# Kernel tuning notes

Hardware: AMD Instinct MI355X
Metric: run time of the kernel (lower is better)

Reference implementation:

```python
import jax, jax.numpy as jnp
import numpy as np

N = 100000
E = 1600000
D_IN = 128
D_OUT = 128

def setup_inputs() -> dict:
    key = jax.random.key(0)
    ks = jax.random.split(key, 8)
    x = jax.random.normal(ks[0], (N, D_IN), dtype=jnp.float32)
    edge_index = jax.random.randint(ks[1], (2, E), 0, N, dtype=jnp.int64)
    s = 1.0 / np.sqrt(D_IN)
    W_l = jax.random.uniform(ks[2], (D_OUT, D_IN), minval=-s, maxval=s, dtype=jnp.float32)
    b_l = jax.random.uniform(ks[3], (D_OUT,), minval=-s, maxval=s, dtype=jnp.float32)
    W_r = jax.random.uniform(ks[4], (D_OUT, D_IN), minval=-s, maxval=s, dtype=jnp.float32)
    gamma = jnp.ones((D_OUT,), dtype=jnp.float32)
    beta = jnp.zeros((D_OUT,), dtype=jnp.float32)
    return {"x": x, "edge_index": edge_index, "W_l": W_l, "b_l": b_l,
            "W_r": W_r, "gamma": gamma, "beta": beta}

def reference(x, edge_index, W_l, b_l, W_r, gamma, beta):
    src, dst = edge_index[0], edge_index[1]
    # mean-aggregate neighbor features: gather src features, scatter-sum to dst
    msg = x[src]                                             # [E, D_IN]
    agg = jax.ops.segment_sum(msg, dst, num_segments=N)      # [N, D_IN]
    deg = jax.ops.segment_sum(jnp.ones((E,), x.dtype), dst, num_segments=N)
    agg = agg / jnp.maximum(deg, 1.0)[:, None]               # nodes w/o neighbors -> 0
    # SAGEConv: lin_l(aggregated) + lin_r(root)
    out = agg @ W_l.T + b_l + x @ W_r.T                      # [N, D_OUT]
    # LayerNorm over feature dim
    mu = jnp.mean(out, axis=-1, keepdims=True)
    var = jnp.var(out, axis=-1, keepdims=True)
    out = (out - mu) * jax.lax.rsqrt(var + 1e-5) * gamma + beta
    # ReLU; dropout in eval mode is identity
    return jax.nn.relu(out)
```

## Files before the change

kernel.cpp:

```cpp
#include <hip/hip_runtime.h>


#define D 128
#define SCAN_NB 256
#define NPB 256
#define MAXNB 1024
#define SLAB 4608
#define NCONV 2048

typedef __attribute__((ext_vector_type(8))) short bf16x8;
typedef __attribute__((ext_vector_type(4))) float f32x4;

__device__ inline unsigned short f2bf(float f) {
    unsigned int u = __builtin_bit_cast(unsigned int, f);
    u += 0x7FFFu + ((u >> 16) & 1u);
    return (unsigned short)(u >> 16);
}
__device__ inline float bf_lo(unsigned int u) {
    return __builtin_bit_cast(float, u << 16);
}
__device__ inline float bf_hi(unsigned int u) {
    return __builtin_bit_cast(float, u & 0xFFFF0000u);
}

__global__ void slab_init(int* __restrict__ bcur, int nb) {
    int b = blockIdx.x * blockDim.x + threadIdx.x;
    if (b < nb) bcur[b] = b * SLAB;
}

__global__ __launch_bounds__(256) void bin_kernel(const int* __restrict__ ei,
                                                  int* __restrict__ bcur,
                                                  unsigned int* __restrict__ staged,
                                                  int n_edges, int nb) {
    __shared__ int hist[MAXNB];
    __shared__ int base[MAXNB];
    int tid = threadIdx.x;
    for (int i = tid; i < nb; i += 256) hist[i] = 0;
    __syncthreads();
    int chunk = (n_edges + gridDim.x - 1) / gridDim.x;
    int e0 = blockIdx.x * chunk, e1 = min(e0 + chunk, n_edges);
    const int* dstp = ei + n_edges;
    for (int e = e0 + tid; e < e1; e += 256)
        atomicAdd(&hist[dstp[e] >> 8], 1);
    __syncthreads();
    for (int i = tid; i < nb; i += 256) {
        int c = hist[i];
        base[i] = c ? atomicAdd(&bcur[i], c) : 0;
        hist[i] = 0;
    }
    __syncthreads();
    for (int e = e0 + tid; e < e1; e += 256) {
        int dst = dstp[e];
        int b = dst >> 8;
        int pos = base[b] + atomicAdd(&hist[b], 1);
        staged[pos] = ((unsigned int)(dst & 255) << 24) | (unsigned int)ei[e];
    }
}

__global__ __launch_bounds__(256) void fill2_slab(const unsigned int* __restrict__ staged,
                                                  const int* __restrict__ bcur,
                                                  int* __restrict__ offs,
                                                  int* __restrict__ deg,
                                                  int* __restrict__ csr, int n_nodes) {
    __shared__ int hist[NPB];
    __shared__ int scn[NPB];
    int b = blockIdx.x;
    int n0 = b << 8;
    int nn = min(NPB, n_nodes - n0);
    int tid = threadIdx.x;
    int base = b * SLAB;
    int cnt = bcur[b] - base;

    hist[tid] = 0;
    __syncthreads();
    for (int e = tid; e < cnt; e += 256)
        atomicAdd(&hist[staged[base + e] >> 24], 1);
    __syncthreads();
    int h = hist[tid];
    scn[tid] = h;
    __syncthreads();
    for (int off = 1; off < 256; off <<= 1) {
        int t = (tid >= off) ? scn[tid - off] : 0;
        __syncthreads();
        scn[tid] += t;
        __syncthreads();
    }
    int start = base + scn[tid] - h;
    if (tid < nn) { offs[n0 + tid] = start; deg[n0 + tid] = h; }
    scn[tid] = start;
    __syncthreads();
    for (int e = tid; e < cnt; e += 256) {
        unsigned int u = staged[base + e];
        int dl = u >> 24;
        int pos = atomicAdd(&scn[dl], 1);
        csr[pos] = (int)(u & 0xFFFFFFu);
    }
}

__global__ __launch_bounds__(256) void prep2_kernel(
        const float* __restrict__ x, unsigned int* __restrict__ xcat, long long n4,
        const float* __restrict__ Wl, const float* __restrict__ Wr,
        bf16x8* __restrict__ wfragg) {
    int b = blockIdx.x;
    int tid = threadIdx.x;
    if (b < NCONV) {
        for (long long i = b * 256LL + tid; i < n4; i += (long long)NCONV * 256) {
            float4 v = reinterpret_cast<const float4*>(x)[i];
            uint2 p;
            p.x = (unsigned int)f2bf(v.x) | ((unsigned int)f2bf(v.y) << 16);
            p.y = (unsigned int)f2bf(v.z) | ((unsigned int)f2bf(v.w) << 16);
            long long row = i >> 5, j = i & 31;
            *reinterpret_cast<uint2*>(xcat + row * 128 + 64 + 2 * j) = p;
        }
    } else {
        int e = (b - NCONV) * 256 + tid;
        int lane = e & 63, kk = (e >> 6) & 7, n0 = e >> 9;
        int dd = n0 * 16 + (lane & 15);
        int k0 = kk * 32 + 8 * (lane >> 4);
        bf16x8 v;
        #pragma unroll
        for (int j = 0; j < 8; ++j) {
            int k = k0 + j;
            float w = (k < 128) ? Wl[dd * 128 + k] : Wr[dd * 128 + (k - 128)];
            v[j] = (short)f2bf(w);
        }
        wfragg[e] = v;
    }
}

__global__ void gather4_kernel(unsigned int* __restrict__ xcat,
                               const int* __restrict__ offs,
                               const int* __restrict__ deg,
                               const int* __restrict__ csr, int n_nodes) {
    int lane = threadIdx.x & 63;
    int col = lane & 15;
    int q   = lane >> 4;
    int gw = (blockIdx.x * blockDim.x + threadIdx.x) >> 6;
    int nw = (gridDim.x * blockDim.x) >> 6;

    for (int node = gw; node < n_nodes; node += nw) {
        int o0 = offs[node], dgi = deg[node], o1 = o0 + dgi;
        float a0 = 0.f, a1 = 0.f, a2 = 0.f, a3 = 0.f,
              a4 = 0.f, a5 = 0.f, a6 = 0.f, a7 = 0.f;
        int i = o0 + q;
        #define LROW(s) (*reinterpret_cast<const uint4*>(xcat + (size_t)(s) * 128 + 64 + (col << 2)))
        #define ACC(u) do { \
            a0 += bf_lo((u).x); a1 += bf_hi((u).x); \
            a2 += bf_lo((u).y); a3 += bf_hi((u).y); \
            a4 += bf_lo((u).z); a5 += bf_hi((u).z); \
            a6 += bf_lo((u).w); a7 += bf_hi((u).w); } while (0)
        for (; i + 12 < o1; i += 16) {
            int s0 = csr[i], s1 = csr[i + 4], s2 = csr[i + 8], s3 = csr[i + 12];
            uint4 u0 = LROW(s0), u1 = LROW(s1), u2 = LROW(s2), u3 = LROW(s3);
            ACC(u0); ACC(u1); ACC(u2); ACC(u3);
        }
        for (; i + 4 < o1; i += 8) {
            int s0 = csr[i], s1 = csr[i + 4];
            uint4 u0 = LROW(s0), u1 = LROW(s1);
            ACC(u0); ACC(u1);
        }
        for (; i < o1; i += 4) {
            uint4 u0 = LROW(csr[i]);
            ACC(u0);
        }
        #undef ACC
        #undef LROW
        a0 += __shfl_xor(a0, 16, 64); a0 += __shfl_xor(a0, 32, 64);
        a1 += __shfl_xor(a1, 16, 64); a1 += __shfl_xor(a1, 32, 64);
        a2 += __shfl_xor(a2, 16, 64); a2 += __shfl_xor(a2, 32, 64);
        a3 += __shfl_xor(a3, 16, 64); a3 += __shfl_xor(a3, 32, 64);
        a4 += __shfl_xor(a4, 16, 64); a4 += __shfl_xor(a4, 32, 64);
        a5 += __shfl_xor(a5, 16, 64); a5 += __shfl_xor(a5, 32, 64);
        a6 += __shfl_xor(a6, 16, 64); a6 += __shfl_xor(a6, 32, 64);
        a7 += __shfl_xor(a7, 16, 64); a7 += __shfl_xor(a7, 32, 64);
        if (q == 0) {
            float inv = 1.0f / fmaxf((float)dgi, 1.0f);
            uint4 p;
            p.x = (unsigned int)f2bf(a0 * inv) | ((unsigned int)f2bf(a1 * inv) << 16);
            p.y = (unsigned int)f2bf(a2 * inv) | ((unsigned int)f2bf(a3 * inv) << 16);
            p.z = (unsigned int)f2bf(a4 * inv) | ((unsigned int)f2bf(a5 * inv) << 16);
            p.w = (unsigned int)f2bf(a6 * inv) | ((unsigned int)f2bf(a7 * inv) << 16);
            *reinterpret_cast<uint4*>(xcat + (size_t)node * 128 + (col << 2)) = p;
        }
    }
}

__global__ __launch_bounds__(256) void sage_mfma3(
        const unsigned int* __restrict__ xcat,
        const bf16x8* __restrict__ wfragg,
        const float* __restrict__ bl,
        const float* __restrict__ gamma,
        const float* __restrict__ beta,
        float* __restrict__ out,
        int n_nodes) {
    __shared__ bf16x8 wf[8 * 8 * 64];

    int tid = threadIdx.x;
    #pragma unroll
    for (int i = 0; i < 16; ++i) wf[i * 256 + tid] = wfragg[i * 256 + tid];
    __syncthreads();

    int wave = tid >> 6, lane = tid & 63;
    int sl = lane & 15, g = lane >> 4;
    int gw = blockIdx.x * 4 + wave;
    int nw = gridDim.x * 4;
    int ndt = (n_nodes + 31) >> 5;

    for (int t = gw; t < ndt; t += nw) {
        int R0 = t << 5;
        int nodeA = R0 + sl;       if (nodeA >= n_nodes) nodeA = n_nodes - 1;
        int nodeB = R0 + 16 + sl;  if (nodeB >= n_nodes) nodeB = n_nodes - 1;
        const bf16x8* arA = reinterpret_cast<const bf16x8*>(xcat) + (size_t)nodeA * 32;
        const bf16x8* arB = reinterpret_cast<const bf16x8*>(xcat) + (size_t)nodeB * 32;

        f32x4 accA[8], accB[8];
        #pragma unroll
        for (int n0 = 0; n0 < 8; ++n0) {
            accA[n0] = (f32x4){0.f, 0.f, 0.f, 0.f};
            accB[n0] = (f32x4){0.f, 0.f, 0.f, 0.f};
        }

        #pragma unroll
        for (int ph = 0; ph < 2; ++ph) {
            bf16x8 vaA[4], vaB[4];
            #pragma unroll
            for (int kk = 0; kk < 4; ++kk) {
                vaA[kk] = arA[ph * 16 + kk * 4 + g];
                vaB[kk] = arB[ph * 16 + kk * 4 + g];
            }
            #pragma unroll
            for (int n0 = 0; n0 < 8; ++n0)
                #pragma unroll
                for (int kk = 0; kk < 4; ++kk) {
                    bf16x8 w = wf[(n0 * 8 + ph * 4 + kk) * 64 + lane];
                    accA[n0] = __builtin_amdgcn_mfma_f32_16x16x32_bf16(vaA[kk], w, accA[n0], 0, 0, 0);
                    accB[n0] = __builtin_amdgcn_mfma_f32_16x16x32_bf16(vaB[kk], w, accB[n0], 0, 0, 0);
                }
        }

        #pragma unroll
        for (int half = 0; half < 2; ++half) {
            f32x4* acc = half ? accB : accA;
            int Rb = R0 + half * 16;
            float s[4] = {0.f, 0.f, 0.f, 0.f}, sq[4] = {0.f, 0.f, 0.f, 0.f};
            #pragma unroll
            for (int n0 = 0; n0 < 8; ++n0) {
                float blv = bl[n0 * 16 + sl];
                #pragma unroll
                for (int r = 0; r < 4; ++r) {
                    float v = acc[n0][r] + blv;
                    acc[n0][r] = v;
                    s[r] += v; sq[r] += v * v;
                }
            }
            #pragma unroll
            for (int off = 1; off <= 8; off <<= 1) {
                #pragma unroll
                for (int r = 0; r < 4; ++r) {
                    s[r]  += __shfl_xor(s[r], off, 64);
                    sq[r] += __shfl_xor(sq[r], off, 64);
                }
            }
            float mu[4], rstd[4];
            #pragma unroll
            for (int r = 0; r < 4; ++r) {
                mu[r] = s[r] * (1.0f / 128.0f);
                float var = sq[r] * (1.0f / 128.0f) - mu[r] * mu[r];
                rstd[r] = rsqrtf(var + 1e-5f);
            }
            #pragma unroll
            for (int n0 = 0; n0 < 8; ++n0) {
                float gm = gamma[n0 * 16 + sl];
                float bt = beta[n0 * 16 + sl];
                #pragma unroll
                for (int r = 0; r < 4; ++r) {
                    int m = Rb + 4 * g + r;
                    if (m < n_nodes) {
                        float o = (acc[n0][r] - mu[r]) * rstd[r] * gm + bt;
                        out[(size_t)m * 128 + n0 * 16 + sl] = fmaxf(o, 0.0f);
                    }
                }
            }
        }
    }
}

__global__ void count_kernel(const int* __restrict__ ei, int* __restrict__ deg, int n_edges) {
    for (int e = blockIdx.x * blockDim.x + threadIdx.x; e < n_edges;
         e += gridDim.x * blockDim.x)
        atomicAdd(&deg[ei[n_edges + e]], 1);
}
__global__ __launch_bounds__(256) void scan_partA(const int* __restrict__ deg,
                                                  int* __restrict__ bsum, int n) {
    __shared__ int red[256];
    int b = blockIdx.x;
    int chunk = (n + SCAN_NB - 1) / SCAN_NB;
    int s0 = b * chunk, s1 = min(s0 + chunk, n);
    int sum = 0;
    for (int i = s0 + threadIdx.x; i < s1; i += 256) sum += deg[i];
    red[threadIdx.x] = sum;
    __syncthreads();
    for (int off = 128; off >= 1; off >>= 1) {
        if (threadIdx.x < off) red[threadIdx.x] += red[threadIdx.x + off];
        __syncthreads();
    }
    if (threadIdx.x == 0) bsum[b] = red[0];
}
__global__ __launch_bounds__(SCAN_NB) void scan_partB(const int* __restrict__ bsum,
                                                      int* __restrict__ boff,
                                                      int* __restrict__ offs, int n) {
    __shared__ int tmp[SCAN_NB];
    int tid = threadIdx.x;
    int v = bsum[tid];
    tmp[tid] = v;
    __syncthreads();
    for (int off = 1; off < SCAN_NB; off <<= 1) {
        int t = (tid >= off) ? tmp[tid - off] : 0;
        __syncthreads();
        tmp[tid] += t;
        __syncthreads();
    }
    boff[tid] = tmp[tid] - v;
    if (tid == SCAN_NB - 1) offs[n] = tmp[tid];
}
__global__ __launch_bounds__(256) void scan_partC(const int* __restrict__ deg,
                                                  const int* __restrict__ boff,
                                                  int* __restrict__ offs,
                                                  int* __restrict__ cursor, int n) {
    __shared__ int tsum[256];
    int b = blockIdx.x;
    int chunk = (n + SCAN_NB - 1) / SCAN_NB;
    int s0 = b * chunk, s1 = min(s0 + chunk, n);
    int tchunk = (chunk + 255) >> 8;
    int t0 = s0 + threadIdx.x * tchunk;
    int t1 = min(t0 + tchunk, s1);
    int sum = 0;
    for (int i = t0; i < t1; ++i) sum += deg[i];
    tsum[threadIdx.x] = sum;
    __syncthreads();
    for (int off = 1; off < 256; off <<= 1) {
        int t = (threadIdx.x >= off) ? tsum[threadIdx.x - off] : 0;
        __syncthreads();
        tsum[threadIdx.x] += t;
        __syncthreads();
    }
    int run = boff[b] + tsum[threadIdx.x] - sum;
    for (int i = t0; i < t1; ++i) {
        offs[i] = run; cursor[i] = run; run += deg[i];
    }
}
__global__ void fill_kernel(const int* __restrict__ ei, int* __restrict__ cursor,
                            int* __restrict__ csr, int n_edges) {
    for (int e = blockIdx.x * blockDim.x + threadIdx.x; e < n_edges;
         e += gridDim.x * blockDim.x) {
        int src = ei[e];
        int dst = ei[n_edges + e];
        int pos = atomicAdd(&cursor[dst], 1);
        csr[pos] = src;
    }
}
__global__ void degfix_kernel(const int* __restrict__ offs, int* __restrict__ deg, int n) {
    for (int i = blockIdx.x * blockDim.x + threadIdx.x; i < n;
         i += gridDim.x * blockDim.x)
        deg[i] = offs[i + 1] - offs[i];
}

__global__ void zero_f(float* __restrict__ a, float* __restrict__ dg, int n_nodes) {
    int total = n_nodes * D + n_nodes;
    for (int i = blockIdx.x * blockDim.x + threadIdx.x; i < total;
         i += gridDim.x * blockDim.x) {
        if (i < n_nodes * D) a[i] = 0.0f;
        else                 dg[i - n_nodes * D] = 0.0f;
    }
}
__global__ void scatter_kernel(const float* __restrict__ x, const int* __restrict__ ei,
                               float* __restrict__ agg, float* __restrict__ deg, int n_edges) {
    long long total = (long long)n_edges * 32;
    for (long long idx = blockIdx.x * (long long)blockDim.x + threadIdx.x; idx < total;
         idx += (long long)gridDim.x * blockDim.x) {
        int e = (int)(idx >> 5);
        int j = (int)(idx & 31);
        int src = ei[e];
        int dst = ei[n_edges + e];
        float4 v = reinterpret_cast<const float4*>(x)[(long long)src * 32 + j];
        float* a = agg + (long long)dst * D + j * 4;
        atomicAdd(a + 0, v.x); atomicAdd(a + 1, v.y);
        atomicAdd(a + 2, v.z); atomicAdd(a + 3, v.w);
        if (j == 0) atomicAdd(deg + dst, 1.0f);
    }
}
__global__ __launch_bounds__(1024) void sage_scalar(
        const float* __restrict__ x, const float* __restrict__ agg_in,
        const float* __restrict__ deg,
        const float* __restrict__ Wl, const float* __restrict__ bl,
        const float* __restrict__ Wr,
        const float* __restrict__ gamma, const float* __restrict__ beta,
        float* __restrict__ out, int n_nodes) {
    __shared__ float wlt[128 * 129];
    __shared__ float wrt[128 * 129];
    __shared__ float rows[16][256];
    int tid = threadIdx.x;
    for (int i = tid; i < 128 * 128; i += 1024) {
        int d = i >> 7, k = i & 127;
        wlt[k * 129 + d] = Wl[i];
        wrt[k * 129 + d] = Wr[i];
    }
    __syncthreads();
    int wave = tid >> 6, lane = tid & 63;
    int gwave = blockIdx.x * 16 + wave;
    int nwaves = gridDim.x * 16;
    float* row = rows[wave];
    int d0 = lane, d1 = lane + 64;
    float bl0 = bl[d0], bl1 = bl[d1];
    float g0 = gamma[d0], g1 = gamma[d1];
    float be0 = beta[d0], be1 = beta[d1];
    for (int n = gwave; n < n_nodes; n += nwaves) {
        float inv = 1.0f / fmaxf(deg[n], 1.0f);
        long long base = (long long)n * D;
        row[lane]       = agg_in[base + lane] * inv;
        row[lane + 64]  = agg_in[base + lane + 64] * inv;
        row[lane + 128] = x[base + lane];
        row[lane + 192] = x[base + lane + 64];
        float acc0 = bl0, acc1 = bl1;
        #pragma unroll 4
        for (int k = 0; k < 128; ++k) {
            float a  = row[k];
            float xv = row[128 + k];
            acc0 += a * wlt[k * 129 + d0];
            acc1 += a * wlt[k * 129 + d1];
            acc0 += xv * wrt[k * 129 + d0];
            acc1 += xv * wrt[k * 129 + d1];
        }
        float s  = acc0 + acc1;
        float sq = acc0 * acc0 + acc1 * acc1;
        #pragma unroll
        for (int off = 32; off >= 1; off >>= 1) {
            s  += __shfl_xor(s, off, 64);
            sq += __shfl_xor(sq, off, 64);
        }
        float mu = s * (1.0f / 128.0f);
        float var = sq * (1.0f / 128.0f) - mu * mu;
        float rstd = rsqrtf(var + 1e-5f);
        float o0 = (acc0 - mu) * rstd * g0 + be0;
        float o1 = (acc1 - mu) * rstd * g1 + be1;
        out[base + d0] = fmaxf(o0, 0.0f);
        out[base + d1] = fmaxf(o1, 0.0f);
    }
}

extern "C" void kernel_launch(void* const* d_in, const int* in_sizes, int n_in,
                              void* d_out, int out_size, void* d_ws, size_t ws_size,
                              hipStream_t stream) {
    const float* x     = (const float*)d_in[0];
    const int*   ei    = (const int*)d_in[1];
    const float* Wl    = (const float*)d_in[2];
    const float* bl    = (const float*)d_in[3];
    const float* Wr    = (const float*)d_in[4];
    const float* gamma = (const float*)d_in[5];
    const float* beta  = (const float*)d_in[6];

    int n_nodes = in_sizes[0] / D;
    int n_edges = in_sizes[1] / 2;
    int nb = (n_nodes + NPB - 1) / NPB;
    int ndt = (n_nodes + 31) >> 5;
    int sage_blocks = (ndt + 3) / 4;

    size_t csr_slab  = (size_t)nb * SLAB;
    size_t csr_leg   = (size_t)n_edges;
    size_t head      = (size_t)n_nodes * 3 + 1 + 2 * SCAN_NB + MAXNB + 16384;
    size_t int_slab  = (head + (csr_slab > csr_leg ? csr_slab : csr_leg)) * sizeof(int);
    size_t int_leg   = (head + csr_leg) * sizeof(int);
    size_t xc_off_s  = (int_slab + 255) & ~(size_t)255;
    size_t xc_off_l  = (int_leg + 255) & ~(size_t)255;
    size_t xcat_b    = (size_t)n_nodes * 256 * 2;
    size_t need_slab = xc_off_s + xcat_b;
    size_t need_leg  = xc_off_l + xcat_b;

    int* deg    = (int*)d_ws;
    int* offs   = deg + n_nodes;
    int* cursor = offs + n_nodes + 1;
    int* bsum   = cursor + n_nodes;
    int* boff   = bsum + SCAN_NB;
    int* bcur   = boff + SCAN_NB;
    int* wfrag  = bcur + MAXNB;
    int* csr    = wfrag + 16384;

    bool slab_ok = (nb <= MAXNB) && (n_nodes < (1 << 24)) &&
                   (csr_slab * 4 <= xcat_b) && (ws_size >= need_slab);

    if (slab_ok) {
        unsigned int* xcat = (unsigned int*)((char*)d_ws + xc_off_s);
        unsigned int* staged = xcat;

        slab_init<<<(nb + 255) / 256, 256, 0, stream>>>(bcur, nb);
        bin_kernel<<<512, 256, 0, stream>>>(ei, bcur, staged, n_edges, nb);
        fill2_slab<<<nb, 256, 0, stream>>>(staged, bcur, offs, deg, csr, n_nodes);
        prep2_kernel<<<NCONV + 16, 256, 0, stream>>>(
            x, xcat, (long long)n_nodes * 32, Wl, Wr, (bf16x8*)wfrag);
        gather4_kernel<<<2048, 256, 0, stream>>>(xcat, offs, deg, csr, n_nodes);
        sage_mfma3<<<sage_blocks, 256, 0, stream>>>(xcat, (const bf16x8*)wfrag, bl,
                                                    gamma, beta, (float*)d_out, n_nodes);
    } else if (ws_size >= need_leg && n_nodes < (1 << 24)) {
        unsigned int* xcat = (unsigned int*)((char*)d_ws + xc_off_l);

        hipMemsetAsync(deg, 0, (size_t)n_nodes * sizeof(int), stream);
        count_kernel<<<2048, 256, 0, stream>>>(ei, deg, n_edges);
        scan_partA<<<SCAN_NB, 256, 0, stream>>>(deg, bsum, n_nodes);
        scan_partB<<<1, SCAN_NB, 0, stream>>>(bsum, boff, offs, n_nodes);
        scan_partC<<<SCAN_NB, 256, 0, stream>>>(deg, boff, offs, cursor, n_nodes);
        fill_kernel<<<2048, 256, 0, stream>>>(ei, cursor, csr, n_edges);
        degfix_kernel<<<256, 256, 0, stream>>>(offs, deg, n_nodes);
        prep2_kernel<<<NCONV + 16, 256, 0, stream>>>(
            x, xcat, (long long)n_nodes * 32, Wl, Wr, (bf16x8*)wfrag);
        gather4_kernel<<<2048, 256, 0, stream>>>(xcat, offs, deg, csr, n_nodes);
        sage_mfma3<<<sage_blocks, 256, 0, stream>>>(xcat, (const bf16x8*)wfrag, bl,
                                                    gamma, beta, (float*)d_out, n_nodes);
    } else {
        float* degf = (float*)d_ws;
        zero_f<<<2048, 256, 0, stream>>>((float*)d_out, degf, n_nodes);
        scatter_kernel<<<2048, 256, 0, stream>>>(x, ei, (float*)d_out, degf, n_edges);
        sage_scalar<<<512, 1024, 0, stream>>>(x, (float*)d_out, degf, Wl, bl, Wr,
                                              gamma, beta, (float*)d_out, n_nodes);
    }
}
```

Measured before the change: 160.0 us.

## Gather four nodes per wave and double sage block size

The gather kernel now assigns one node to each 16-lane quarter-wave, so a wave handles four nodes at once. This removes the cross-quarter shuffle reduction and the single-lane store, but each quarter now walks its node's whole edge list serially with 2-way unrolling, and the four nodes may have different degrees. The MFMA SAGE kernel moves to 512-thread blocks with 8 waves, which halves the per-block weight-fragment staging into shared memory relative to the work done. When the node count is not a multiple of four, the clamped tail node is written redundantly by several quarters.

```diff
diff --git a/kernel.cpp b/kernel.cpp
--- a/kernel.cpp
+++ b/kernel.cpp
@@ -128,7 +128,7 @@
     }
 }
 
-__global__ void gather4_kernel(unsigned int* __restrict__ xcat,
+__global__ void gather5_kernel(unsigned int* __restrict__ xcat,
                                const int* __restrict__ offs,
                                const int* __restrict__ deg,
                                const int* __restrict__ csr, int n_nodes) {
@@ -137,55 +137,43 @@
     int q   = lane >> 4;
     int gw = (blockIdx.x * blockDim.x + threadIdx.x) >> 6;
     int nw = (gridDim.x * blockDim.x) >> 6;
-
-    for (int node = gw; node < n_nodes; node += nw) {
+    int ngroups = (n_nodes + 3) >> 2;
+
+    for (int grp = gw; grp < ngroups; grp += nw) {
+        int node = grp * 4 + q;
+        if (node >= n_nodes) node = n_nodes - 1;
         int o0 = offs[node], dgi = deg[node], o1 = o0 + dgi;
         float a0 = 0.f, a1 = 0.f, a2 = 0.f, a3 = 0.f,
               a4 = 0.f, a5 = 0.f, a6 = 0.f, a7 = 0.f;
-        int i = o0 + q;
         #define LROW(s) (*reinterpret_cast<const uint4*>(xcat + (size_t)(s) * 128 + 64 + (col << 2)))
         #define ACC(u) do { \
             a0 += bf_lo((u).x); a1 += bf_hi((u).x); \
             a2 += bf_lo((u).y); a3 += bf_hi((u).y); \
             a4 += bf_lo((u).z); a5 += bf_hi((u).z); \
             a6 += bf_lo((u).w); a7 += bf_hi((u).w); } while (0)
-        for (; i + 12 < o1; i += 16) {
-            int s0 = csr[i], s1 = csr[i + 4], s2 = csr[i + 8], s3 = csr[i + 12];
-            uint4 u0 = LROW(s0), u1 = LROW(s1), u2 = LROW(s2), u3 = LROW(s3);
-            ACC(u0); ACC(u1); ACC(u2); ACC(u3);
-        }
-        for (; i + 4 < o1; i += 8) {
-            int s0 = csr[i], s1 = csr[i + 4];
+        int i = o0;
+        for (; i + 1 < o1; i += 2) {
+            int s0 = csr[i], s1 = csr[i + 1];
             uint4 u0 = LROW(s0), u1 = LROW(s1);
             ACC(u0); ACC(u1);
         }
-        for (; i < o1; i += 4) {
+        if (i < o1) {
             uint4 u0 = LROW(csr[i]);
             ACC(u0);
         }
         #undef ACC
         #undef LROW
-        a0 += __shfl_xor(a0, 16, 64); a0 += __shfl_xor(a0, 32, 64);
-        a1 += __shfl_xor(a1, 16, 64); a1 += __shfl_xor(a1, 32, 64);
-        a2 += __shfl_xor(a2, 16, 64); a2 += __shfl_xor(a2, 32, 64);
-        a3 += __shfl_xor(a3, 16, 64); a3 += __shfl_xor(a3, 32, 64);
-        a4 += __shfl_xor(a4, 16, 64); a4 += __shfl_xor(a4, 32, 64);
-        a5 += __shfl_xor(a5, 16, 64); a5 += __shfl_xor(a5, 32, 64);
-        a6 += __shfl_xor(a6, 16, 64); a6 += __shfl_xor(a6, 32, 64);
-        a7 += __shfl_xor(a7, 16, 64); a7 += __shfl_xor(a7, 32, 64);
-        if (q == 0) {
-            float inv = 1.0f / fmaxf((float)dgi, 1.0f);
-            uint4 p;
-            p.x = (unsigned int)f2bf(a0 * inv) | ((unsigned int)f2bf(a1 * inv) << 16);
-            p.y = (unsigned int)f2bf(a2 * inv) | ((unsigned int)f2bf(a3 * inv) << 16);
-            p.z = (unsigned int)f2bf(a4 * inv) | ((unsigned int)f2bf(a5 * inv) << 16);
-            p.w = (unsigned int)f2bf(a6 * inv) | ((unsigned int)f2bf(a7 * inv) << 16);
-            *reinterpret_cast<uint4*>(xcat + (size_t)node * 128 + (col << 2)) = p;
-        }
-    }
-}
-
-__global__ __launch_bounds__(256) void sage_mfma3(
+        float inv = 1.0f / fmaxf((float)dgi, 1.0f);
+        uint4 p;
+        p.x = (unsigned int)f2bf(a0 * inv) | ((unsigned int)f2bf(a1 * inv) << 16);
+        p.y = (unsigned int)f2bf(a2 * inv) | ((unsigned int)f2bf(a3 * inv) << 16);
+        p.z = (unsigned int)f2bf(a4 * inv) | ((unsigned int)f2bf(a5 * inv) << 16);
+        p.w = (unsigned int)f2bf(a6 * inv) | ((unsigned int)f2bf(a7 * inv) << 16);
+        *reinterpret_cast<uint4*>(xcat + (size_t)node * 128 + (col << 2)) = p;
+    }
+}
+
+__global__ __launch_bounds__(512) void sage_mfma4(
         const unsigned int* __restrict__ xcat,
         const bf16x8* __restrict__ wfragg,
         const float* __restrict__ bl,
@@ -197,13 +185,13 @@
 
     int tid = threadIdx.x;
     #pragma unroll
-    for (int i = 0; i < 16; ++i) wf[i * 256 + tid] = wfragg[i * 256 + tid];
+    for (int i = 0; i < 8; ++i) wf[i * 512 + tid] = wfragg[i * 512 + tid];
     __syncthreads();
 
     int wave = tid >> 6, lane = tid & 63;
     int sl = lane & 15, g = lane >> 4;
-    int gw = blockIdx.x * 4 + wave;
-    int nw = gridDim.x * 4;
+    int gw = blockIdx.x * 8 + wave;
+    int nw = gridDim.x * 8;
     int ndt = (n_nodes + 31) >> 5;
 
     for (int t = gw; t < ndt; t += nw) {
@@ -463,7 +451,7 @@
     int n_edges = in_sizes[1] / 2;
     int nb = (n_nodes + NPB - 1) / NPB;
     int ndt = (n_nodes + 31) >> 5;
-    int sage_blocks = (ndt + 3) / 4;
+    int sage_blocks = (ndt + 7) / 8;
 
     size_t csr_slab  = (size_t)nb * SLAB;
     size_t csr_leg   = (size_t)n_edges;
@@ -497,8 +485,8 @@
         fill2_slab<<<nb, 256, 0, stream>>>(staged, bcur, offs, deg, csr, n_nodes);
         prep2_kernel<<<NCONV + 16, 256, 0, stream>>>(
             x, xcat, (long long)n_nodes * 32, Wl, Wr, (bf16x8*)wfrag);
-        gather4_kernel<<<2048, 256, 0, stream>>>(xcat, offs, deg, csr, n_nodes);
-        sage_mfma3<<<sage_blocks, 256, 0, stream>>>(xcat, (const bf16x8*)wfrag, bl,
+        gather5_kernel<<<2048, 256, 0, stream>>>(xcat, offs, deg, csr, n_nodes);
+        sage_mfma4<<<sage_blocks, 512, 0, stream>>>(xcat, (const bf16x8*)wfrag, bl,
                                                     gamma, beta, (float*)d_out, n_nodes);
     } else if (ws_size >= need_leg && n_nodes < (1 << 24)) {
         unsigned int* xcat = (unsigned int*)((char*)d_ws + xc_off_l);
@@ -512,8 +500,8 @@
         degfix_kernel<<<256, 256, 0, stream>>>(offs, deg, n_nodes);
         prep2_kernel<<<NCONV + 16, 256, 0, stream>>>(
             x, xcat, (long long)n_nodes * 32, Wl, Wr, (bf16x8*)wfrag);
-        gather4_kernel<<<2048, 256, 0, stream>>>(xcat, offs, deg, csr, n_nodes);
-        sage_mfma3<<<sage_blocks, 256, 0, stream>>>(xcat, (const bf16x8*)wfrag, bl,
+        gather5_kernel<<<2048, 256, 0, stream>>>(xcat, offs, deg, csr, n_nodes);
+        sage_mfma4<<<sage_blocks, 512, 0, stream>>>(xcat, (const bf16x8*)wfrag, bl,
                                                     gamma, beta, (float*)d_out, n_nodes);
     } else {
         float* degf = (float*)d_ws;
```

Result: slower. 199.6 us (+24.8%).
